# Kernel optimization log

Hardware: AMD Instinct MI355X
Metric: run time of the kernel (lower is better)

Reference implementation:

```python
import jax, jax.numpy as jnp
import numpy as np

N, C, H, W = 2, 128, 64, 64
N_HEAD = 4
GROUPS = 16
EPS = 1e-5


def group_norm(x, scale, offset):
    # haiku GroupNorm, channels_first: normalize over (channels-in-group, h, w)
    n, c, h, w = x.shape
    xg = x.reshape(n, GROUPS, c // GROUPS, h, w)
    mu = xg.mean(axis=(2, 3, 4), keepdims=True)
    var = xg.var(axis=(2, 3, 4), keepdims=True)
    xg = (xg - mu) * jax.lax.rsqrt(var + EPS)
    return xg.reshape(n, c, h, w) * scale[None, :, None, None] + offset[None, :, None, None]


def setup_inputs() -> dict:
    key = jax.random.key(0)
    ks = jax.random.split(key, 4)
    inv_sqrt_c = 1.0 / np.sqrt(C).astype(np.float32)
    return {
        "x": jax.random.normal(ks[0], (N, C, H, W), dtype=jnp.float32),
        "w_qkv": jax.random.normal(ks[1], (C, 3 * C), dtype=jnp.float32) * inv_sqrt_c,
        "b_qkv": jnp.zeros((3 * C,), dtype=jnp.float32),
        "w_out": jax.random.normal(ks[2], (C, C), dtype=jnp.float32) * inv_sqrt_c,
        "b_out": jnp.zeros((C,), dtype=jnp.float32),
        "gn1_scale": jnp.ones((C,), dtype=jnp.float32),
        "gn1_offset": jnp.zeros((C,), dtype=jnp.float32),
        "gn2_scale": jnp.ones((C,), dtype=jnp.float32),
        "gn2_offset": jnp.zeros((C,), dtype=jnp.float32),
    }


def reference(x, w_qkv, b_qkv, w_out, b_out, gn1_scale, gn1_offset, gn2_scale, gn2_offset):
    n, c, h, w = x.shape
    dh = c // N_HEAD
    # GroupNorm (x is reassigned, so the residual uses the normalized x)
    xn = group_norm(x, gn1_scale, gn1_offset)
    # 1x1 conv qkv projection: [n, 3c, h, w]
    qkv = jnp.einsum('nchw,cd->ndhw', xn, w_qkv) + b_qkv[None, :, None, None]
    # [n, 3H, dh, hw] -> [n, 3H, hw, dh]
    qkv = jnp.swapaxes(qkv.reshape(n, N_HEAD * 3, dh, h * w), 2, 3)
    q, k, v = jnp.split(qkv, 3, axis=1)  # each [n, H, hw, dh]
    scale = dh ** (-0.25)
    # [n, H, hw, hw] attention matrix (the memory-bound core)
    att = jax.nn.softmax((q * scale) @ (jnp.swapaxes(k, 2, 3) * scale), axis=3)
    y = jnp.swapaxes(att @ v, 2, 3).reshape(n, c, h, w)
    # 1x1 conv out projection + GroupNorm + residual
    out = jnp.einsum('nchw,cd->ndhw', y, w_out) + b_out[None, :, None, None]
    return xn + group_norm(out, gn2_scale, gn2_offset)
```

## Files before the change

kernel.cpp:

```cpp
#include <hip/hip_runtime.h>
#include <hip/hip_bf16.h>
#include <math.h>

constexpr int cHW   = 4096;
constexpr int cC    = 128;
constexpr int cNH   = 4;
constexpr int cDH   = 32;
constexpr float cEPS = 1e-5f;
constexpr float cQS = 0.2550347805f;
constexpr int SPLIT = 4;

typedef short bh8  __attribute__((ext_vector_type(8)));
typedef float f4   __attribute__((ext_vector_type(4)));
typedef float f16a __attribute__((ext_vector_type(16)));

static __device__ __forceinline__ unsigned short f2bf(float f) {
  union { __hip_bfloat16 h; unsigned short u; } cv;
  cv.h = __float2bfloat16(f);
  return cv.u;
}
static __device__ __forceinline__ unsigned pack2bf(float a, float b) {
  return (unsigned)f2bf(a) | ((unsigned)f2bf(b) << 16);
}
static __device__ __forceinline__ unsigned pack_trunc(float a, float b) {
  unsigned ua = __builtin_bit_cast(unsigned, a);
  unsigned ub = __builtin_bit_cast(unsigned, b);
  return (ua >> 16) | (ub & 0xffff0000u);
}
static __device__ __forceinline__ float bflo(unsigned pk) {
  return __builtin_bit_cast(float, pk << 16);
}
static __device__ __forceinline__ float bfhi(unsigned pk) {
  return __builtin_bit_cast(float, pk & 0xffff0000u);
}
static __device__ __forceinline__ void plswap(unsigned& a, unsigned& b) {
#if __has_builtin(__builtin_amdgcn_permlane32_swap)
  typedef int v2i __attribute__((ext_vector_type(2)));
  v2i r = __builtin_amdgcn_permlane32_swap((int)a, (int)b, false, false);
  a = (unsigned)r[0]; b = (unsigned)r[1];
#else
  asm("v_permlane32_swap_b32 %0, %1" : "+v"(a), "+v"(b));
#endif
}
static __device__ __forceinline__ bh8 mk8(unsigned a, unsigned b, unsigned c, unsigned d) {
  union { unsigned u[4]; bh8 v; } t;
  t.u[0] = a; t.u[1] = b; t.u[2] = c; t.u[3] = d;
  return t.v;
}

__device__ __forceinline__ void block_reduce2(float& a, float& b, float* sbuf) {
  #pragma unroll
  for (int off = 32; off > 0; off >>= 1) {
    a += __shfl_down(a, off, 64);
    b += __shfl_down(b, off, 64);
  }
  int wave = threadIdx.x >> 6;
  int lane = threadIdx.x & 63;
  if (lane == 0) { sbuf[wave] = a; sbuf[4 + wave] = b; }
  __syncthreads();
  if (threadIdx.x == 0) {
    sbuf[8] = sbuf[0] + sbuf[1] + sbuf[2] + sbuf[3];
    sbuf[9] = sbuf[4] + sbuf[5] + sbuf[6] + sbuf[7];
  }
  __syncthreads();
  a = sbuf[8];
  b = sbuf[9];
}

__global__ __launch_bounds__(256)
void prep(const float* __restrict__ x, float* __restrict__ part,
          const float* __restrict__ wq, const float* __restrict__ wo,
          unsigned short* __restrict__ wqT, unsigned short* __restrict__ woT) {
  __shared__ float lds[32 * 133];
  int L = threadIdx.x;
  if (blockIdx.x < 256) {
    int ng = blockIdx.x >> 3, sl = blockIdx.x & 7;
    const float4* s4 = (const float4*)x;
    float s = 0.f, s2 = 0.f;
    #pragma unroll
    for (int i = 0; i < 4; i++) {
      int idx = i * 256 + L;
      int c = idx >> 7, tt = idx & 127;
      float4 v = s4[(size_t)(ng * 8 + c) * 1024 + sl * 128 + tt];
      s  += v.x + v.y + v.z + v.w;
      s2 += v.x*v.x + v.y*v.y + v.z*v.z + v.w*v.w;
    }
    block_reduce2(s, s2, lds);
    if (L == 0) { part[blockIdx.x * 2] = s; part[blockIdx.x * 2 + 1] = s2; }
  } else {
    int bx = blockIdx.x - 256;
    const float* src; unsigned short* dst; int W, d0;
    if (bx < 12) { src = wq; dst = wqT; W = 384; d0 = bx * 32; }
    else         { src = wo; dst = woT; W = 128; d0 = (bx - 12) * 32; }
    #pragma unroll
    for (int i = 0; i < 16; i++) {
      int c = i * 8 + (L >> 5), d = L & 31;
      lds[d * 133 + c] = src[(size_t)c * W + d0 + d];
    }
    __syncthreads();
    int d = L >> 3, ch = L & 7, c0 = ch * 16;
    unsigned pk[8];
    #pragma unroll
    for (int j = 0; j < 8; j++)
      pk[j] = pack2bf(lds[d * 133 + c0 + 2 * j], lds[d * 133 + c0 + 2 * j + 1]);
    uint4* d4 = (uint4*)(dst + (size_t)(d0 + d) * 128 + c0);
    d4[0] = make_uint4(pk[0], pk[1], pk[2], pk[3]);
    d4[1] = make_uint4(pk[4], pk[5], pk[6], pk[7]);
  }
}

__global__ __launch_bounds__(256)
void gn_stats(const float* __restrict__ src, float* __restrict__ part) {
  __shared__ float sbuf[10];
  int ng = blockIdx.x >> 3, sl = blockIdx.x & 7;
  const float4* s4 = (const float4*)src;
  float s = 0.f, s2 = 0.f;
  #pragma unroll
  for (int i = 0; i < 4; i++) {
    int idx = i * 256 + threadIdx.x;
    int c = idx >> 7, tt = idx & 127;
    float4 v = s4[(size_t)(ng * 8 + c) * 1024 + sl * 128 + tt];
    s  += v.x + v.y + v.z + v.w;
    s2 += v.x*v.x + v.y*v.y + v.z*v.z + v.w*v.w;
  }
  block_reduce2(s, s2, sbuf);
  if (threadIdx.x == 0) { part[blockIdx.x * 2] = s; part[blockIdx.x * 2 + 1] = s2; }
}

__global__ __launch_bounds__(256)
void gn1_pack(const float* __restrict__ x, const float* __restrict__ part,
              const float* __restrict__ sc, const float* __restrict__ of,
              unsigned short* __restrict__ xnB) {
  int cc = blockIdx.x, ts = blockIdx.y, n = blockIdx.z;
  int ng = n * 16 + cc;
  float s = 0.f, s2 = 0.f;
  #pragma unroll
  for (int p = 0; p < 8; p++) { s += part[(ng*8+p)*2]; s2 += part[(ng*8+p)*2+1]; }
  float mu = s * (1.0f / 32768.0f);
  float rinv = rsqrtf(s2 * (1.0f / 32768.0f) - mu * mu + cEPS);
  int t = ts * 256 + threadIdx.x;
  float v[8];
  #pragma unroll
  for (int j = 0; j < 8; j++) {
    int c = cc * 8 + j;
    float a = rinv * sc[c];
    float bo = of[c] - mu * a;
    v[j] = x[((size_t)n * cC + c) * cHW + t] * a + bo;
  }
  unsigned pk[4];
  #pragma unroll
  for (int j = 0; j < 4; j++) pk[j] = pack2bf(v[2*j], v[2*j+1]);
  ((uint4*)xnB)[(size_t)(n * 16 + cc) * cHW + t] = make_uint4(pk[0], pk[1], pk[2], pk[3]);
}

__global__ __launch_bounds__(256)
void qkv_mfma(const unsigned short* __restrict__ xnB, const unsigned short* __restrict__ wqT,
              const float* __restrict__ bq, unsigned* __restrict__ qF,
              unsigned* __restrict__ kF, unsigned* __restrict__ vF) {
  __shared__ float vbuf[64 * 36];
  const int L = threadIdx.x & 63, w = threadIdx.x >> 6;
  const int c16 = L & 15, q = L >> 4;
  const int t0 = blockIdx.x * 64, dg = blockIdx.y, n = blockIdx.z;
  const int nh = n * 4 + (dg & 3), d0 = dg * 32;
  const f4 zf = {0.f, 0.f, 0.f, 0.f};
  f4 acc0 = zf, acc1 = zf;
  const int trow = t0 + w * 16 + c16;
  #pragma unroll
  for (int ks = 0; ks < 4; ks++) {
    bh8 a  = *(const bh8*)(xnB + ((size_t)(n * 16 + ks * 4 + q) * cHW + trow) * 8);
    bh8 b0 = *(const bh8*)(wqT + (size_t)(d0 + c16) * 128 + ks * 32 + q * 8);
    bh8 b1 = *(const bh8*)(wqT + (size_t)(d0 + 16 + c16) * 128 + ks * 32 + q * 8);
    acc0 = __builtin_amdgcn_mfma_f32_16x16x32_bf16(a, b0, acc0, 0, 0, 0);
    acc1 = __builtin_amdgcn_mfma_f32_16x16x32_bf16(a, b1, acc1, 0, 0, 0);
  }
  const float blo = bq[d0 + c16], bhi = bq[d0 + 16 + c16];
  const float scl = (dg < 4) ? cQS : 1.0f;
  #pragma unroll
  for (int r = 0; r < 4; r++) {
    vbuf[(w * 16 + q * 4 + r) * 36 + c16]      = (acc0[r] + blo) * scl;
    vbuf[(w * 16 + q * 4 + r) * 36 + 16 + c16] = (acc1[r] + bhi) * scl;
  }
  __syncthreads();
  const int tl = threadIdx.x >> 7, fr = (threadIdx.x >> 6) & 1, LL = threadIdx.x & 63;
  const int col = LL & 31, h2 = LL >> 5;
  unsigned pk[4];
  if (dg < 8) {
    const float* src = &vbuf[(tl * 32 + col) * 36 + fr * 16 + h2 * 8];
    #pragma unroll
    for (int jj = 0; jj < 4; jj++) pk[jj] = pack2bf(src[2 * jj], src[2 * jj + 1]);
  } else {
    const float* src = &vbuf[(tl * 32 + fr * 16 + h2 * 8) * 36 + col];
    #pragma unroll
    for (int jj = 0; jj < 4; jj++) pk[jj] = pack2bf(src[2 * jj * 36], src[(2 * jj + 1) * 36]);
  }
  unsigned* dst = (dg < 4) ? qF : ((dg < 8) ? kF : vF);
  size_t frag = ((size_t)(nh * 128 + (t0 >> 5) + tl) * 2 + fr) * 64 + LL;
  ((uint4*)dst)[frag] = make_uint4(pk[0], pk[1], pk[2], pk[3]);
}

__global__ __launch_bounds__(128, 4)
void flash_mfma(const unsigned short* __restrict__ qF,
                const unsigned short* __restrict__ kF,
                const unsigned short* __restrict__ vF,
                unsigned* __restrict__ opart, float* __restrict__ lpart) {
  const int w = threadIdx.x >> 6, L = threadIdx.x & 63;
  const int col = L & 31, hi = L >> 5;
  const int qt = blockIdx.x * 2 + w, nh = blockIdx.y, ph = blockIdx.z;
  const short oneb = 0x3F80;
  const bh8 ones = {oneb, oneb, oneb, oneb, oneb, oneb, oneb, oneb};
  const f16a zf16 = {0.f,0.f,0.f,0.f, 0.f,0.f,0.f,0.f, 0.f,0.f,0.f,0.f, 0.f,0.f,0.f,0.f};

  const unsigned short* qb = qF + ((size_t)(nh * 128 + qt) * 2) * 512;
  bh8 qf0 = *(const bh8*)(qb + L * 8);
  bh8 qf1 = *(const bh8*)(qb + 512 + L * 8);

  const unsigned short* kb = kF + (size_t)nh * 128 * 1024;
  const unsigned short* vb = vF + (size_t)nh * 128 * 1024;

  f16a o = zf16, lacc = zf16;

  const int tb0 = ph * (cHW / SPLIT / 32);
  #pragma unroll 2
  for (int tl = tb0; tl < tb0 + (cHW / SPLIT / 32); ++tl) {
    const unsigned short* kp = kb + (size_t)tl * 1024;
    const unsigned short* vp = vb + (size_t)tl * 1024;
    bh8 ka0 = *(const bh8*)(kp + L * 8);
    bh8 ka1 = *(const bh8*)(kp + 512 + L * 8);
    bh8 vfa = *(const bh8*)(vp + L * 8);
    bh8 vfb = *(const bh8*)(vp + 512 + L * 8);
    f16a s = __builtin_amdgcn_mfma_f32_32x32x16_bf16(ka0, qf0, zf16, 0, 0, 0);
    s = __builtin_amdgcn_mfma_f32_32x32x16_bf16(ka1, qf1, s, 0, 0, 0);
    #pragma unroll
    for (int r = 0; r < 16; r++) s[r] = __builtin_amdgcn_exp2f(s[r]);
    unsigned pk0 = pack_trunc(s[0],  s[1]);
    unsigned pk1 = pack_trunc(s[2],  s[3]);
    unsigned pk2 = pack_trunc(s[4],  s[5]);
    unsigned pk3 = pack_trunc(s[6],  s[7]);
    unsigned pk4 = pack_trunc(s[8],  s[9]);
    unsigned pk5 = pack_trunc(s[10], s[11]);
    unsigned pk6 = pack_trunc(s[12], s[13]);
    unsigned pk7 = pack_trunc(s[14], s[15]);
    plswap(pk0, pk2); plswap(pk1, pk3);
    plswap(pk4, pk6); plswap(pk5, pk7);
    bh8 pf0 = mk8(pk0, pk1, pk2, pk3);
    bh8 pf1 = mk8(pk4, pk5, pk6, pk7);
    o    = __builtin_amdgcn_mfma_f32_32x32x16_bf16(pf0, vfa,  o,    0, 0, 0);
    lacc = __builtin_amdgcn_mfma_f32_32x32x16_bf16(pf0, ones, lacc, 0, 0, 0);
    o    = __builtin_amdgcn_mfma_f32_32x32x16_bf16(pf1, vfb,  o,    0, 0, 0);
    lacc = __builtin_amdgcn_mfma_f32_32x32x16_bf16(pf1, ones, lacc, 0, 0, 0);
  }

  const size_t base = (size_t)ph * 32768 + (size_t)nh * cHW + (size_t)qt * 32;
  #pragma unroll
  for (int k = 0; k < 8; k++) {
    const int rowlo = ((2 * k) & 3) + 8 * (k >> 1) + 4 * hi;
    opart[((base + rowlo) >> 1) * 32 + col] = pack_trunc(o[2 * k], o[2 * k + 1]);
  }
  if (col == 0) {
    #pragma unroll
    for (int r = 0; r < 16; r++)
      lpart[base + (r & 3) + 8 * (r >> 2) + 4 * hi] = lacc[r];
  }
}

__global__ __launch_bounds__(256)
void combine(const unsigned* __restrict__ opart, const float* __restrict__ lpart,
             unsigned* __restrict__ yB) {
  int tid = blockIdx.x * 256 + threadIdx.x;
  size_t rp = (size_t)(tid >> 1);
  int h = tid & 1;
  size_t r0 = rp * 2;
  float l0 = 0.f, l1 = 0.f;
  #pragma unroll
  for (int p = 0; p < SPLIT; p++) {
    l0 += lpart[(size_t)p * 32768 + r0];
    l1 += lpart[(size_t)p * 32768 + r0 + 1];
  }
  float e0[16], e1[16];
  #pragma unroll
  for (int j = 0; j < 16; j++) { e0[j] = 0.f; e1[j] = 0.f; }
  #pragma unroll
  for (int p = 0; p < SPLIT; p++) {
    const uint4* op = (const uint4*)(opart + ((size_t)p * 16384 + rp) * 32 + h * 16);
    #pragma unroll
    for (int j = 0; j < 4; j++) {
      uint4 v = op[j];
      e0[j*4+0] += bflo(v.x); e1[j*4+0] += bfhi(v.x);
      e0[j*4+1] += bflo(v.y); e1[j*4+1] += bfhi(v.y);
      e0[j*4+2] += bflo(v.z); e1[j*4+2] += bfhi(v.z);
      e0[j*4+3] += bflo(v.w); e1[j*4+3] += bfhi(v.w);
    }
  }
  float i0 = 1.0f / l0, i1 = 1.0f / l1;
  unsigned pkA[8], pkB[8];
  #pragma unroll
  for (int j = 0; j < 8; j++) {
    pkA[j] = pack2bf(e0[2*j] * i0, e0[2*j+1] * i0);
    pkB[j] = pack2bf(e1[2*j] * i1, e1[2*j+1] * i1);
  }
  uint4* dA = (uint4*)(yB + r0 * 16 + h * 8);
  dA[0] = make_uint4(pkA[0], pkA[1], pkA[2], pkA[3]);
  dA[1] = make_uint4(pkA[4], pkA[5], pkA[6], pkA[7]);
  uint4* dB = (uint4*)(yB + (r0 + 1) * 16 + h * 8);
  dB[0] = make_uint4(pkB[0], pkB[1], pkB[2], pkB[3]);
  dB[1] = make_uint4(pkB[4], pkB[5], pkB[6], pkB[7]);
}

__global__ __launch_bounds__(256)
void out_mfma(const unsigned short* __restrict__ yB, const unsigned short* __restrict__ woT,
              const float* __restrict__ bo, float* __restrict__ proj) {
  __shared__ float obuf[64 * 36];
  const int L = threadIdx.x & 63, w = threadIdx.x >> 6;
  const int c16 = L & 15, q = L >> 4;
  const int t0 = blockIdx.x * 64, d0 = blockIdx.y * 32, n = blockIdx.z;
  const f4 zf = {0.f, 0.f, 0.f, 0.f};
  f4 acc0 = zf, acc1 = zf;
  const int trow = t0 + w * 16 + c16;
  #pragma unroll
  for (int h = 0; h < 4; h++) {
    bh8 a  = *(const bh8*)(yB + ((size_t)(n * 4 + h) * cHW + trow) * 32 + q * 8);
    bh8 b0 = *(const bh8*)(woT + (size_t)(d0 + c16) * 128 + h * 32 + q * 8);
    bh8 b1 = *(const bh8*)(woT + (size_t)(d0 + 16 + c16) * 128 + h * 32 + q * 8);
    acc0 = __builtin_amdgcn_mfma_f32_16x16x32_bf16(a, b0, acc0, 0, 0, 0);
    acc1 = __builtin_amdgcn_mfma_f32_16x16x32_bf16(a, b1, acc1, 0, 0, 0);
  }
  float blo = bo[d0 + c16], bhi = bo[d0 + 16 + c16];
  #pragma unroll
  for (int r = 0; r < 4; r++) {
    obuf[(w * 16 + q * 4 + r) * 36 + c16]      = acc0[r] + blo;
    obuf[(w * 16 + q * 4 + r) * 36 + 16 + c16] = acc1[r] + bhi;
  }
  __syncthreads();
  int t16 = threadIdx.x & 15, d8 = (threadIdx.x >> 4) & 15;
  #pragma unroll
  for (int tc = 0; tc < 4; tc++)
    #pragma unroll
    for (int hh = 0; hh < 2; hh++) {
      int d = d8 + hh * 16;
      proj[((size_t)n * cC + d0 + d) * cHW + t0 + tc * 16 + t16] =
          obuf[(tc * 16 + t16) * 36 + d];
    }
}

__global__ __launch_bounds__(256)
void gn2_apply(const float* __restrict__ x, const float* __restrict__ proj,
               const float* __restrict__ p1, const float* __restrict__ p2,
               const float* __restrict__ s1, const float* __restrict__ o1,
               const float* __restrict__ s2, const float* __restrict__ o2,
               float* __restrict__ out) {
  int tid = blockIdx.x * 256 + threadIdx.x;
  int Cg = tid >> 8;
  int n = Cg >> 7, ch = Cg & 127, g = ch >> 3, ng = n * 16 + g;
  float sa = 0.f, sb = 0.f, ta = 0.f, tb = 0.f;
  #pragma unroll
  for (int p = 0; p < 8; p++) {
    sa += p1[(ng*8+p)*2]; sb += p1[(ng*8+p)*2+1];
    ta += p2[(ng*8+p)*2]; tb += p2[(ng*8+p)*2+1];
  }
  float mu1 = sa * (1.0f/32768.0f);
  float ri1 = rsqrtf(sb * (1.0f/32768.0f) - mu1*mu1 + cEPS);
  float a1 = ri1 * s1[ch], b1 = o1[ch] - mu1 * a1;
  float mu2 = ta * (1.0f/32768.0f);
  float ri2 = rsqrtf(tb * (1.0f/32768.0f) - mu2*mu2 + cEPS);
  float a2 = ri2 * s2[ch], b2 = o2[ch] - mu2 * a2;
  const float4* x4 = (const float4*)x;
  const float4* pr4 = (const float4*)proj;
  float4* o4 = (float4*)out;
  #pragma unroll
  for (int i = 0; i < 4; i++) {
    size_t f = (size_t)tid * 4 + i;
    float4 xv = x4[f], pv = pr4[f];
    float4 r;
    r.x = xv.x * a1 + b1 + pv.x * a2 + b2;
    r.y = xv.y * a1 + b1 + pv.y * a2 + b2;
    r.z = xv.z * a1 + b1 + pv.z * a2 + b2;
    r.w = xv.w * a1 + b1 + pv.w * a2 + b2;
    o4[f] = r;
  }
}

extern "C" void kernel_launch(void* const* d_in, const int* in_sizes, int n_in,
                              void* d_out, int out_size, void* d_ws, size_t ws_size,
                              hipStream_t stream) {
  const float* x     = (const float*)d_in[0];
  const float* w_qkv = (const float*)d_in[1];
  const float* b_qkv = (const float*)d_in[2];
  const float* w_out = (const float*)d_in[3];
  const float* b_out = (const float*)d_in[4];
  const float* g1s   = (const float*)d_in[5];
  const float* g1o   = (const float*)d_in[6];
  const float* g2s   = (const float*)d_in[7];
  const float* g2o   = (const float*)d_in[8];
  float* out = (float*)d_out;
  float* ws  = (float*)d_ws;

  const size_t MAP = (size_t)2 * cC * cHW;
  float* proj    = ws;
  float* lpart   = proj + MAP;
  float* stats1  = lpart + (size_t)SPLIT * 32768;
  float* stats2  = stats1 + 512;
  unsigned* opart = (unsigned*)(stats2 + 512);
  unsigned* qF   = opart + (size_t)SPLIT * 32768 * 16;
  unsigned* kF   = qF + MAP / 2;
  unsigned* vF   = kF + MAP / 2;
  unsigned* yB   = vF + MAP / 2;
  unsigned short* xnB = (unsigned short*)(yB + MAP / 2);
  unsigned short* wqT = xnB + MAP;
  unsigned short* woT = wqT + 49152;

  prep      <<<dim3(272),           256, 0, stream>>>(x, stats1, w_qkv, w_out, wqT, woT);
  gn1_pack  <<<dim3(16, 16, 2),     256, 0, stream>>>(x, stats1, g1s, g1o, xnB);
  qkv_mfma  <<<dim3(64, 12, 2),     256, 0, stream>>>(xnB, wqT, b_qkv, qF, kF, vF);
  flash_mfma<<<dim3(64, 8, SPLIT),  128, 0, stream>>>((const unsigned short*)qF,
                                                      (const unsigned short*)kF,
                                                      (const unsigned short*)vF,
                                                      opart, lpart);
  combine   <<<dim3(128),           256, 0, stream>>>(opart, lpart, yB);
  out_mfma  <<<dim3(64, 4, 2),      256, 0, stream>>>((const unsigned short*)yB, woT,
                                                      b_out, proj);
  gn_stats  <<<dim3(256),           256, 0, stream>>>(proj, stats2);
  gn2_apply <<<dim3(256),           256, 0, stream>>>(x, proj, stats1, stats2,
                                                      g1s, g1o, g2s, g2o, out);
}
```

Measured before the change: 130.1 us.

## Fuse GN2 stats into out projection via atomics; two query tiles per flash wave

```diff
diff --git a/kernel.cpp b/kernel.cpp
--- a/kernel.cpp
+++ b/kernel.cpp
@@ -70,7 +70,8 @@
 __global__ __launch_bounds__(256)
 void prep(const float* __restrict__ x, float* __restrict__ part,
           const float* __restrict__ wq, const float* __restrict__ wo,
-          unsigned short* __restrict__ wqT, unsigned short* __restrict__ woT) {
+          unsigned short* __restrict__ wqT, unsigned short* __restrict__ woT,
+          float* __restrict__ stats2) {
   __shared__ float lds[32 * 133];
   int L = threadIdx.x;
   if (blockIdx.x < 256) {
@@ -89,6 +90,7 @@
     if (L == 0) { part[blockIdx.x * 2] = s; part[blockIdx.x * 2 + 1] = s2; }
   } else {
     int bx = blockIdx.x - 256;
+    if (bx == 0 && L < 64) stats2[L] = 0.f;
     const float* src; unsigned short* dst; int W, d0;
     if (bx < 12) { src = wq; dst = wqT; W = 384; d0 = bx * 32; }
     else         { src = wo; dst = woT; W = 128; d0 = (bx - 12) * 32; }
@@ -107,24 +109,6 @@
     d4[0] = make_uint4(pk[0], pk[1], pk[2], pk[3]);
     d4[1] = make_uint4(pk[4], pk[5], pk[6], pk[7]);
   }
-}
-
-__global__ __launch_bounds__(256)
-void gn_stats(const float* __restrict__ src, float* __restrict__ part) {
-  __shared__ float sbuf[10];
-  int ng = blockIdx.x >> 3, sl = blockIdx.x & 7;
-  const float4* s4 = (const float4*)src;
-  float s = 0.f, s2 = 0.f;
-  #pragma unroll
-  for (int i = 0; i < 4; i++) {
-    int idx = i * 256 + threadIdx.x;
-    int c = idx >> 7, tt = idx & 127;
-    float4 v = s4[(size_t)(ng * 8 + c) * 1024 + sl * 128 + tt];
-    s  += v.x + v.y + v.z + v.w;
-    s2 += v.x*v.x + v.y*v.y + v.z*v.z + v.w*v.w;
-  }
-  block_reduce2(s, s2, sbuf);
-  if (threadIdx.x == 0) { part[blockIdx.x * 2] = s; part[blockIdx.x * 2 + 1] = s2; }
 }
 
 __global__ __launch_bounds__(256)
@@ -198,29 +182,31 @@
   ((uint4*)dst)[frag] = make_uint4(pk[0], pk[1], pk[2], pk[3]);
 }
 
-__global__ __launch_bounds__(128, 4)
+__global__ __launch_bounds__(128, 2)
 void flash_mfma(const unsigned short* __restrict__ qF,
                 const unsigned short* __restrict__ kF,
                 const unsigned short* __restrict__ vF,
                 unsigned* __restrict__ opart, float* __restrict__ lpart) {
   const int w = threadIdx.x >> 6, L = threadIdx.x & 63;
   const int col = L & 31, hi = L >> 5;
-  const int qt = blockIdx.x * 2 + w, nh = blockIdx.y, ph = blockIdx.z;
+  const int qt0 = blockIdx.x * 4 + w * 2;
+  const int nh = blockIdx.y, ph = blockIdx.z;
   const short oneb = 0x3F80;
   const bh8 ones = {oneb, oneb, oneb, oneb, oneb, oneb, oneb, oneb};
   const f16a zf16 = {0.f,0.f,0.f,0.f, 0.f,0.f,0.f,0.f, 0.f,0.f,0.f,0.f, 0.f,0.f,0.f,0.f};
 
-  const unsigned short* qb = qF + ((size_t)(nh * 128 + qt) * 2) * 512;
-  bh8 qf0 = *(const bh8*)(qb + L * 8);
-  bh8 qf1 = *(const bh8*)(qb + 512 + L * 8);
+  const unsigned short* qb = qF + ((size_t)(nh * 128 + qt0) * 2) * 512;
+  bh8 qfA0 = *(const bh8*)(qb + L * 8);
+  bh8 qfA1 = *(const bh8*)(qb + 512 + L * 8);
+  bh8 qfB0 = *(const bh8*)(qb + 1024 + L * 8);
+  bh8 qfB1 = *(const bh8*)(qb + 1536 + L * 8);
 
   const unsigned short* kb = kF + (size_t)nh * 128 * 1024;
   const unsigned short* vb = vF + (size_t)nh * 128 * 1024;
 
-  f16a o = zf16, lacc = zf16;
+  f16a oA = zf16, lA = zf16, oB = zf16, lB = zf16;
 
   const int tb0 = ph * (cHW / SPLIT / 32);
-  #pragma unroll 2
   for (int tl = tb0; tl < tb0 + (cHW / SPLIT / 32); ++tl) {
     const unsigned short* kp = kb + (size_t)tl * 1024;
     const unsigned short* vp = vb + (size_t)tl * 1024;
@@ -228,38 +214,68 @@
     bh8 ka1 = *(const bh8*)(kp + 512 + L * 8);
     bh8 vfa = *(const bh8*)(vp + L * 8);
     bh8 vfb = *(const bh8*)(vp + 512 + L * 8);
-    f16a s = __builtin_amdgcn_mfma_f32_32x32x16_bf16(ka0, qf0, zf16, 0, 0, 0);
-    s = __builtin_amdgcn_mfma_f32_32x32x16_bf16(ka1, qf1, s, 0, 0, 0);
-    #pragma unroll
-    for (int r = 0; r < 16; r++) s[r] = __builtin_amdgcn_exp2f(s[r]);
-    unsigned pk0 = pack_trunc(s[0],  s[1]);
-    unsigned pk1 = pack_trunc(s[2],  s[3]);
-    unsigned pk2 = pack_trunc(s[4],  s[5]);
-    unsigned pk3 = pack_trunc(s[6],  s[7]);
-    unsigned pk4 = pack_trunc(s[8],  s[9]);
-    unsigned pk5 = pack_trunc(s[10], s[11]);
-    unsigned pk6 = pack_trunc(s[12], s[13]);
-    unsigned pk7 = pack_trunc(s[14], s[15]);
-    plswap(pk0, pk2); plswap(pk1, pk3);
-    plswap(pk4, pk6); plswap(pk5, pk7);
-    bh8 pf0 = mk8(pk0, pk1, pk2, pk3);
-    bh8 pf1 = mk8(pk4, pk5, pk6, pk7);
-    o    = __builtin_amdgcn_mfma_f32_32x32x16_bf16(pf0, vfa,  o,    0, 0, 0);
-    lacc = __builtin_amdgcn_mfma_f32_32x32x16_bf16(pf0, ones, lacc, 0, 0, 0);
-    o    = __builtin_amdgcn_mfma_f32_32x32x16_bf16(pf1, vfb,  o,    0, 0, 0);
-    lacc = __builtin_amdgcn_mfma_f32_32x32x16_bf16(pf1, ones, lacc, 0, 0, 0);
-  }
-
-  const size_t base = (size_t)ph * 32768 + (size_t)nh * cHW + (size_t)qt * 32;
-  #pragma unroll
-  for (int k = 0; k < 8; k++) {
-    const int rowlo = ((2 * k) & 3) + 8 * (k >> 1) + 4 * hi;
-    opart[((base + rowlo) >> 1) * 32 + col] = pack_trunc(o[2 * k], o[2 * k + 1]);
-  }
-  if (col == 0) {
-    #pragma unroll
-    for (int r = 0; r < 16; r++)
-      lpart[base + (r & 3) + 8 * (r >> 2) + 4 * hi] = lacc[r];
+
+    {
+      f16a s = __builtin_amdgcn_mfma_f32_32x32x16_bf16(ka0, qfA0, zf16, 0, 0, 0);
+      s = __builtin_amdgcn_mfma_f32_32x32x16_bf16(ka1, qfA1, s, 0, 0, 0);
+      #pragma unroll
+      for (int r = 0; r < 16; r++) s[r] = __builtin_amdgcn_exp2f(s[r]);
+      unsigned pk0 = pack_trunc(s[0],  s[1]);
+      unsigned pk1 = pack_trunc(s[2],  s[3]);
+      unsigned pk2 = pack_trunc(s[4],  s[5]);
+      unsigned pk3 = pack_trunc(s[6],  s[7]);
+      unsigned pk4 = pack_trunc(s[8],  s[9]);
+      unsigned pk5 = pack_trunc(s[10], s[11]);
+      unsigned pk6 = pack_trunc(s[12], s[13]);
+      unsigned pk7 = pack_trunc(s[14], s[15]);
+      plswap(pk0, pk2); plswap(pk1, pk3);
+      plswap(pk4, pk6); plswap(pk5, pk7);
+      bh8 pf0 = mk8(pk0, pk1, pk2, pk3);
+      bh8 pf1 = mk8(pk4, pk5, pk6, pk7);
+      oA = __builtin_amdgcn_mfma_f32_32x32x16_bf16(pf0, vfa,  oA, 0, 0, 0);
+      lA = __builtin_amdgcn_mfma_f32_32x32x16_bf16(pf0, ones, lA, 0, 0, 0);
+      oA = __builtin_amdgcn_mfma_f32_32x32x16_bf16(pf1, vfb,  oA, 0, 0, 0);
+      lA = __builtin_amdgcn_mfma_f32_32x32x16_bf16(pf1, ones, lA, 0, 0, 0);
+    }
+    {
+      f16a s = __builtin_amdgcn_mfma_f32_32x32x16_bf16(ka0, qfB0, zf16, 0, 0, 0);
+      s = __builtin_amdgcn_mfma_f32_32x32x16_bf16(ka1, qfB1, s, 0, 0, 0);
+      #pragma unroll
+      for (int r = 0; r < 16; r++) s[r] = __builtin_amdgcn_exp2f(s[r]);
+      unsigned pk0 = pack_trunc(s[0],  s[1]);
+      unsigned pk1 = pack_trunc(s[2],  s[3]);
+      unsigned pk2 = pack_trunc(s[4],  s[5]);
+      unsigned pk3 = pack_trunc(s[6],  s[7]);
+      unsigned pk4 = pack_trunc(s[8],  s[9]);
+      unsigned pk5 = pack_trunc(s[10], s[11]);
+      unsigned pk6 = pack_trunc(s[12], s[13]);
+      unsigned pk7 = pack_trunc(s[14], s[15]);
+      plswap(pk0, pk2); plswap(pk1, pk3);
+      plswap(pk4, pk6); plswap(pk5, pk7);
+      bh8 pf0 = mk8(pk0, pk1, pk2, pk3);
+      bh8 pf1 = mk8(pk4, pk5, pk6, pk7);
+      oB = __builtin_amdgcn_mfma_f32_32x32x16_bf16(pf0, vfa,  oB, 0, 0, 0);
+      lB = __builtin_amdgcn_mfma_f32_32x32x16_bf16(pf0, ones, lB, 0, 0, 0);
+      oB = __builtin_amdgcn_mfma_f32_32x32x16_bf16(pf1, vfb,  oB, 0, 0, 0);
+      lB = __builtin_amdgcn_mfma_f32_32x32x16_bf16(pf1, ones, lB, 0, 0, 0);
+    }
+  }
+
+  #pragma unroll
+  for (int t = 0; t < 2; t++) {
+    const f16a& o = (t == 0) ? oA : oB;
+    const f16a& l = (t == 0) ? lA : lB;
+    const size_t base = (size_t)ph * 32768 + (size_t)nh * cHW + (size_t)(qt0 + t) * 32;
+    #pragma unroll
+    for (int k = 0; k < 8; k++) {
+      const int rowlo = ((2 * k) & 3) + 8 * (k >> 1) + 4 * hi;
+      opart[((base + rowlo) >> 1) * 32 + col] = pack_trunc(o[2 * k], o[2 * k + 1]);
+    }
+    if (col == 0) {
+      #pragma unroll
+      for (int r = 0; r < 16; r++)
+        lpart[base + (r & 3) + 8 * (r >> 2) + 4 * hi] = l[r];
+    }
   }
 }
 
@@ -308,7 +324,8 @@
 
 __global__ __launch_bounds__(256)
 void out_mfma(const unsigned short* __restrict__ yB, const unsigned short* __restrict__ woT,
-              const float* __restrict__ bo, float* __restrict__ proj) {
+              const float* __restrict__ bo, float* __restrict__ proj,
+              float* __restrict__ stats2) {
   __shared__ float obuf[64 * 36];
   const int L = threadIdx.x & 63, w = threadIdx.x >> 6;
   const int c16 = L & 15, q = L >> 4;
@@ -332,14 +349,31 @@
   }
   __syncthreads();
   int t16 = threadIdx.x & 15, d8 = (threadIdx.x >> 4) & 15;
+  float s[2] = {0.f, 0.f}, s2[2] = {0.f, 0.f};
   #pragma unroll
   for (int tc = 0; tc < 4; tc++)
     #pragma unroll
     for (int hh = 0; hh < 2; hh++) {
       int d = d8 + hh * 16;
-      proj[((size_t)n * cC + d0 + d) * cHW + t0 + tc * 16 + t16] =
-          obuf[(tc * 16 + t16) * 36 + d];
-    }
+      float v = obuf[(tc * 16 + t16) * 36 + d];
+      proj[((size_t)n * cC + d0 + d) * cHW + t0 + tc * 16 + t16] = v;
+      s[hh] += v; s2[hh] += v * v;
+    }
+  #pragma unroll
+  for (int hh = 0; hh < 2; hh++) {
+    float a = s[hh], b = s2[hh];
+    #pragma unroll
+    for (int off = 32; off > 0; off >>= 1) {
+      a += __shfl_down(a, off, 64);
+      b += __shfl_down(b, off, 64);
+    }
+    if (L == 0) {
+      int d = w * 4 + hh * 16;
+      int g = (d0 + d) >> 3;
+      atomicAdd(&stats2[(n * 16 + g) * 2],     a);
+      atomicAdd(&stats2[(n * 16 + g) * 2 + 1], b);
+    }
+  }
 }
 
 __global__ __launch_bounds__(256)
@@ -351,12 +385,12 @@
   int tid = blockIdx.x * 256 + threadIdx.x;
   int Cg = tid >> 8;
   int n = Cg >> 7, ch = Cg & 127, g = ch >> 3, ng = n * 16 + g;
-  float sa = 0.f, sb = 0.f, ta = 0.f, tb = 0.f;
+  float sa = 0.f, sb = 0.f;
   #pragma unroll
   for (int p = 0; p < 8; p++) {
     sa += p1[(ng*8+p)*2]; sb += p1[(ng*8+p)*2+1];
-    ta += p2[(ng*8+p)*2]; tb += p2[(ng*8+p)*2+1];
-  }
+  }
+  float ta = p2[ng * 2], tb = p2[ng * 2 + 1];
   float mu1 = sa * (1.0f/32768.0f);
   float ri1 = rsqrtf(sb * (1.0f/32768.0f) - mu1*mu1 + cEPS);
   float a1 = ri1 * s1[ch], b1 = o1[ch] - mu1 * a1;
@@ -408,17 +442,17 @@
   unsigned short* wqT = xnB + MAP;
   unsigned short* woT = wqT + 49152;
 
-  prep      <<<dim3(272),           256, 0, stream>>>(x, stats1, w_qkv, w_out, wqT, woT);
+  prep      <<<dim3(272),           256, 0, stream>>>(x, stats1, w_qkv, w_out, wqT, woT,
+                                                      stats2);
   gn1_pack  <<<dim3(16, 16, 2),     256, 0, stream>>>(x, stats1, g1s, g1o, xnB);
   qkv_mfma  <<<dim3(64, 12, 2),     256, 0, stream>>>(xnB, wqT, b_qkv, qF, kF, vF);
-  flash_mfma<<<dim3(64, 8, SPLIT),  128, 0, stream>>>((const unsigned short*)qF,
+  flash_mfma<<<dim3(32, 8, SPLIT),  128, 0, stream>>>((const unsigned short*)qF,
                                                       (const unsigned short*)kF,
                                                       (const unsigned short*)vF,
                                                       opart, lpart);
   combine   <<<dim3(128),           256, 0, stream>>>(opart, lpart, yB);
   out_mfma  <<<dim3(64, 4, 2),      256, 0, stream>>>((const unsigned short*)yB, woT,
-                                                      b_out, proj);
-  gn_stats  <<<dim3(256),           256, 0, stream>>>(proj, stats2);
+                                                      b_out, proj, stats2);
   gn2_apply <<<dim3(256),           256, 0, stream>>>(x, proj, stats1, stats2,
                                                       g1s, g1o, g2s, g2o, out);
 }
```

New measurement: 179.0 us. 1.38x slower.
